# Kernel optimization log

Measured on AMD Instinct MI355X. Metric: run time of the kernel, lower is better.

## Reference

```python
import jax, jax.numpy as jnp
import numpy as np

EMB = 512
N_LAYERS = 8
N_HEADS = 16
FF_MULT = 4
NUM_PATCHES = 196
B = 32
N_VIS = 49
LN_EPS = 1e-5


def _sincos_1d(embed_dim, pos):
    omega = np.arange(embed_dim // 2, dtype=np.float64)
    omega /= embed_dim / 2.0
    omega = 1.0 / 10000 ** omega
    pos = pos.reshape(-1)
    out = np.einsum('m,d->md', pos, omega)
    return np.concatenate([np.sin(out), np.cos(out)], axis=1)


def _sincos_2d(embed_dim, grid_size):
    grid_h = np.arange(grid_size, dtype=np.float32)
    grid_w = np.arange(grid_size, dtype=np.float32)
    grid = np.stack(np.meshgrid(grid_w, grid_h), axis=0).reshape([2, 1, grid_size, grid_size])
    emb_h = _sincos_1d(embed_dim // 2, grid[0])
    emb_w = _sincos_1d(embed_dim // 2, grid[1])
    return np.concatenate([emb_h, emb_w], axis=1)


def setup_inputs() -> dict:
    key = jax.random.key(0)
    ks = jax.random.split(key, 20)
    D, H, FF, L = EMB, N_HEADS, FF_MULT * EMB, N_LAYERS
    s = 0.02
    inp = {}
    inp['x_enc_out_vis'] = jax.random.normal(ks[0], (B, N_VIS + 1, D), dtype=jnp.float32)
    # per-batch permutation of [0, NUM_PATCHES)
    u = jax.random.uniform(ks[1], (B, NUM_PATCHES))
    inp['idx_restore_patches'] = jnp.argsort(u, axis=1).astype(jnp.int32)
    inp['mask_token'] = jax.random.normal(ks[2], (1, 1, D), dtype=jnp.float32) * s
    inp['pos_emb'] = jnp.asarray(_sincos_2d(D, int(NUM_PATCHES ** 0.5))[None], dtype=jnp.float32)
    # stacked per-layer params, layout [in, out] (equivalent to torch Linear math)
    inp['Wq'] = jax.random.normal(ks[3], (L, D, D), dtype=jnp.float32) * s
    inp['bq'] = jnp.zeros((L, D), jnp.float32)
    inp['Wk'] = jax.random.normal(ks[4], (L, D, D), dtype=jnp.float32) * s
    inp['bk'] = jnp.zeros((L, D), jnp.float32)
    inp['Wv'] = jax.random.normal(ks[5], (L, D, D), dtype=jnp.float32) * s
    inp['bv'] = jnp.zeros((L, D), jnp.float32)
    inp['Wo'] = jax.random.normal(ks[6], (L, D, D), dtype=jnp.float32) * s
    inp['bo'] = jnp.zeros((L, D), jnp.float32)
    inp['ln1_g'] = jnp.ones((L, D), jnp.float32)
    inp['ln1_b'] = jnp.zeros((L, D), jnp.float32)
    inp['W1'] = jax.random.normal(ks[7], (L, D, FF), dtype=jnp.float32) * s
    inp['b1'] = jnp.zeros((L, FF), jnp.float32)
    inp['W2'] = jax.random.normal(ks[8], (L, FF, D), dtype=jnp.float32) * s
    inp['b2'] = jnp.zeros((L, D), jnp.float32)
    inp['ln2_g'] = jnp.ones((L, D), jnp.float32)
    inp['ln2_b'] = jnp.zeros((L, D), jnp.float32)
    inp['lnf_g'] = jnp.ones((D,), jnp.float32)
    inp['lnf_b'] = jnp.zeros((D,), jnp.float32)
    return inp


def _layernorm(x, g, b):
    m = jnp.mean(x, axis=-1, keepdims=True)
    v = jnp.mean((x - m) ** 2, axis=-1, keepdims=True)
    return (x - m) * jax.lax.rsqrt(v + LN_EPS) * g + b


def _decoder_forward(x_enc_out_vis, idx_restore, mask_token, pos_emb,
                     Wq, bq, Wk, bk, Wv, bv, Wo, bo, ln1_g, ln1_b,
                     W1, b1, W2, b2, ln2_g, ln2_b, lnf_g, lnf_b):
    Bsz, Nvis1, D = x_enc_out_vis.shape
    N = pos_emb.shape[1]
    H = N_HEADS
    hd = D // H
    # reassemble: visible patches (drop CLS) followed by mask tokens, then unshuffle
    vis = x_enc_out_vis[:, 1:]                                   # [B, Nvis, D]
    mtok = jnp.broadcast_to(mask_token, (Bsz, N - (Nvis1 - 1), D))
    shuffled = jnp.concatenate([vis, mtok], axis=1)              # [B, N, D]
    x = jnp.take_along_axis(shuffled, idx_restore[:, :, None], axis=1) + pos_emb

    def block(x, p):
        wq, bq_, wk, bk_, wv, bv_, wo, bo_, g1, be1, w1, bf1, w2, bf2, g2, be2 = p
        q = (x @ wq + bq_).reshape(Bsz, N, H, hd).transpose(0, 2, 1, 3)
        k = (x @ wk + bk_).reshape(Bsz, N, H, hd).transpose(0, 2, 1, 3)
        v = (x @ wv + bv_).reshape(Bsz, N, H, hd).transpose(0, 2, 1, 3)
        scores = jnp.einsum('bhqd,bhkd->bhqk', q, k) / jnp.sqrt(jnp.float32(hd))
        attn = jax.nn.softmax(scores, axis=-1)
        o = jnp.einsum('bhqk,bhkd->bhqd', attn, v)
        o = o.transpose(0, 2, 1, 3).reshape(Bsz, N, D)
        attended = o @ wo + bo_
        x = _layernorm(attended + x, g1, be1)
        ff = jax.nn.relu(x @ w1 + bf1) @ w2 + bf2
        x = _layernorm(ff + x, g2, be2)
        return x, None

    params = (Wq, bq, Wk, bk, Wv, bv, Wo, bo, ln1_g, ln1_b, W1, b1, W2, b2, ln2_g, ln2_b)
    x, _ = jax.lax.scan(block, x, params)
    return _layernorm(x, lnf_g, lnf_b)


def reference(x_enc_out_vis, idx_restore_patches, mask_token, pos_emb,
              Wq, bq, Wk, bk, Wv, bv, Wo, bo, ln1_g, ln1_b,
              W1, b1, W2, b2, ln2_g, ln2_b, lnf_g, lnf_b):
    return _decoder_forward(x_enc_out_vis, idx_restore_patches, mask_token, pos_emb,
                            Wq, bq, Wk, bk, Wv, bv, Wo, bo, ln1_g, ln1_b,
                            W1, b1, W2, b2, ln2_g, ln2_b, lnf_g, lnf_b)
```

## Files before the change

kernel.cpp:

```cpp
#include <hip/hip_runtime.h>

#define LAYERS 8
#define DIM 512
#define FFD 2048
#define NTOK 6272
#define NSEQ 196
#define BATCH 32
#define NHEAD 16
#define HD 32
#define NP 224
#define PSTRIDE 512

typedef unsigned short u16;
typedef __bf16 bf16x8 __attribute__((ext_vector_type(8)));
typedef float f32x4 __attribute__((ext_vector_type(4)));

__device__ __forceinline__ u16 f2bf(float f) {
    unsigned u = __float_as_uint(f);
    u += 0x7FFF + ((u >> 16) & 1);
    return (u16)(u >> 16);
}

typedef __attribute__((address_space(1))) void gvoid_t;
typedef __attribute__((address_space(3))) void lvoid_t;
__device__ __forceinline__ void gload_lds16(const void* g, void* l) {
    __builtin_amdgcn_global_load_lds((gvoid_t*)g, (lvoid_t*)l, 16, 0, 0);
}

__global__ __launch_bounds__(256) void transpose_w(const float* __restrict__ in,
                                                   u16* __restrict__ out, int K, int N) {
    __shared__ float t[32][33];
    size_t base = (size_t)blockIdx.z * K * N;
    int n0 = blockIdx.x * 32, k0 = blockIdx.y * 32;
    int tx = threadIdx.x, ty = threadIdx.y;
#pragma unroll
    for (int i = 0; i < 4; ++i)
        t[ty + i * 8][tx] = in[base + (size_t)(k0 + ty + i * 8) * N + n0 + tx];
    __syncthreads();
#pragma unroll
    for (int i = 0; i < 4; ++i)
        out[base + (size_t)(n0 + ty + i * 8) * K + k0 + tx] = f2bf(t[tx][ty + i * 8]);
}

__global__ void pack3_bias(const float* __restrict__ a, const float* __restrict__ b,
                           const float* __restrict__ c, float* __restrict__ o, int n) {
    int i = blockIdx.x * 256 + threadIdx.x;
    if (i < n) { o[i] = a[i]; o[n + i] = b[i]; o[2 * n + i] = c[i]; }
}

__global__ __launch_bounds__(128) void gather_pos(const float* __restrict__ xenc,
                                                  const int* __restrict__ idx,
                                                  const float* __restrict__ mtok,
                                                  const float* __restrict__ pos,
                                                  float* __restrict__ x, u16* __restrict__ xb) {
    int token = blockIdx.x;
    int b = token / NSEQ, t = token - b * NSEQ;
    int id = idx[token];
    const float* src = (id < 49) ? (xenc + ((size_t)b * 50 + id + 1) * DIM) : mtok;
    int d = threadIdx.x * 4;
    float4 s = *(const float4*)(src + d);
    float4 p = *(const float4*)(pos + (size_t)t * DIM + d);
    float4 r;
    r.x = s.x + p.x; r.y = s.y + p.y; r.z = s.z + p.z; r.w = s.w + p.w;
    *(float4*)(x + (size_t)token * DIM + d) = r;
    ushort4 rb;
    rb.x = f2bf(r.x); rb.y = f2bf(r.y); rb.z = f2bf(r.z); rb.w = f2bf(r.w);
    *(ushort4*)(xb + (size_t)token * DIM + d) = rb;
}

template<int EPI>
__global__ __launch_bounds__(512) void gemm8(
    const u16* __restrict__ A, int lda, long long zsA,
    const u16* __restrict__ Bt, int ldb, long long zsB,
    const float* __restrict__ bias, long long zsBias,
    float* __restrict__ outF, u16* __restrict__ outB, long long zsOut,
    int N, int K) {
    __shared__ u16 As[128 * 32];
    __shared__ u16 Bs[128 * 32];
    int tid = threadIdx.x;
    int lane = tid & 63, wid = tid >> 6;
    int z = blockIdx.z;
    const u16* Az = A + (size_t)z * zsA;
    const u16* Bz = Bt + (size_t)z * zsB;
    int m0 = blockIdx.y * 128, n0 = blockIdx.x * 128;
    int l16 = lane & 15, kq = lane >> 4;
    int wm = (wid >> 2) * 64, wn = (wid & 3) * 32;
    int arow = tid >> 2, koff0 = (tid & 3) * 16;

    f32x4 acc[4][2];
    f32x4 zero = {0.f, 0.f, 0.f, 0.f};
#pragma unroll
    for (int a = 0; a < 4; ++a)
#pragma unroll
        for (int b = 0; b < 2; ++b) acc[a][b] = zero;

    for (int k0 = 0; k0 < K; k0 += 32) {
        __syncthreads();
        gload_lds16((const char*)Az + ((size_t)(m0 + arow) * lda + k0) * 2 + koff0,
                    (char*)As + (size_t)tid * 16);
        gload_lds16((const char*)Bz + ((size_t)(n0 + arow) * ldb + k0) * 2 + koff0,
                    (char*)Bs + (size_t)tid * 16);
        __syncthreads();

        bf16x8 af[4], bfr[2];
#pragma unroll
        for (int mr = 0; mr < 4; ++mr)
            af[mr] = *(const bf16x8*)&As[(wm + mr * 16 + l16) * 32 + kq * 8];
#pragma unroll
        for (int nc = 0; nc < 2; ++nc)
            bfr[nc] = *(const bf16x8*)&Bs[(wn + nc * 16 + l16) * 32 + kq * 8];
#pragma unroll
        for (int mr = 0; mr < 4; ++mr)
#pragma unroll
            for (int nc = 0; nc < 2; ++nc)
                acc[mr][nc] = __builtin_amdgcn_mfma_f32_16x16x32_bf16(af[mr], bfr[nc],
                                                                      acc[mr][nc], 0, 0, 0);
    }

    const float* biasz = (EPI != 4) ? bias + (size_t)z * zsBias : nullptr;
#pragma unroll
    for (int mr = 0; mr < 4; ++mr)
#pragma unroll
        for (int nc = 0; nc < 2; ++nc)
#pragma unroll
            for (int i = 0; i < 4; ++i) {
                int rg = m0 + wm + mr * 16 + kq * 4 + i;
                int cg = n0 + wn + nc * 16 + l16;
                float v = acc[mr][nc][i];
                size_t off = (size_t)z * zsOut + (size_t)rg * N + cg;
                if (EPI == 1) { v += biasz[cg]; outB[off] = f2bf(v > 0.f ? v : 0.f); }
                else if (EPI == 3) { v += biasz[cg]; outB[off] = f2bf(v); }
                else outF[off] = v;
            }
}

__global__ __launch_bounds__(256) void red_ln(const float* __restrict__ p0, long long ps,
                                              const float* __restrict__ bias,
                                              const float* __restrict__ gg,
                                              const float* __restrict__ bb,
                                              float* __restrict__ x, u16* __restrict__ xb) {
    int t = blockIdx.x * 4 + (threadIdx.x >> 6);
    int lane = threadIdx.x & 63;
    size_t base = (size_t)t * DIM;
    int c0 = lane * 4, c1 = 256 + lane * 4;
    float4 a = *(const float4*)(p0 + base + c0);
    float4 c = *(const float4*)(p0 + base + c1);
    float4 a2 = *(const float4*)(p0 + ps + base + c0);
    float4 c2 = *(const float4*)(p0 + ps + base + c1);
    float4 ba = *(const float4*)(bias + c0);
    float4 bc = *(const float4*)(bias + c1);
    float4 xa = *(const float4*)(x + base + c0);
    float4 xc = *(const float4*)(x + base + c1);
    a.x += a2.x + ba.x + xa.x; a.y += a2.y + ba.y + xa.y;
    a.z += a2.z + ba.z + xa.z; a.w += a2.w + ba.w + xa.w;
    c.x += c2.x + bc.x + xc.x; c.y += c2.y + bc.y + xc.y;
    c.z += c2.z + bc.z + xc.z; c.w += c2.w + bc.w + xc.w;
    float s = a.x + a.y + a.z + a.w + c.x + c.y + c.z + c.w;
    float s2 = a.x * a.x + a.y * a.y + a.z * a.z + a.w * a.w
             + c.x * c.x + c.y * c.y + c.z * c.z + c.w * c.w;
#pragma unroll
    for (int off = 32; off; off >>= 1) { s += __shfl_xor(s, off); s2 += __shfl_xor(s2, off); }
    float m = s * (1.f / 512.f);
    float var = s2 * (1.f / 512.f) - m * m;
    float rs = rsqrtf(var + 1e-5f);
    float4 g0 = *(const float4*)(gg + c0);
    float4 g1 = *(const float4*)(gg + c1);
    float4 b0 = *(const float4*)(bb + c0);
    float4 b1 = *(const float4*)(bb + c1);
    float4 o0, o1;
    o0.x = (a.x - m) * rs * g0.x + b0.x;
    o0.y = (a.y - m) * rs * g0.y + b0.y;
    o0.z = (a.z - m) * rs * g0.z + b0.z;
    o0.w = (a.w - m) * rs * g0.w + b0.w;
    o1.x = (c.x - m) * rs * g1.x + b1.x;
    o1.y = (c.y - m) * rs * g1.y + b1.y;
    o1.z = (c.z - m) * rs * g1.z + b1.z;
    o1.w = (c.w - m) * rs * g1.w + b1.w;
    *(float4*)(x + base + c0) = o0;
    *(float4*)(x + base + c1) = o1;
    ushort4 u0, u1;
    u0.x = f2bf(o0.x); u0.y = f2bf(o0.y); u0.z = f2bf(o0.z); u0.w = f2bf(o0.w);
    u1.x = f2bf(o1.x); u1.y = f2bf(o1.y); u1.z = f2bf(o1.z); u1.w = f2bf(o1.w);
    *(ushort4*)(xb + base + c0) = u0;
    *(ushort4*)(xb + base + c1) = u1;
}

__global__ __launch_bounds__(256) void attn_mfma(const u16* __restrict__ qkvb,
                                                 u16* __restrict__ ob) {
    __shared__ u16 Ks[NP * 32];
    __shared__ u16 VTs[32 * 232];
    __shared__ u16 Ps[4][16 * (PSTRIDE / 2)];
    int bh = blockIdx.x;
    int b = bh >> 4, h = bh & 15;
    int tid = threadIdx.x, lane = tid & 63, wid = tid >> 6;
    int l16 = lane & 15, kq = lane >> 4;
    const size_t MS = (size_t)NTOK * DIM;
    const u16* qg = qkvb + ((size_t)b * NSEQ) * DIM + h * HD;
    const u16* kg = qg + MS;
    const u16* vg = qg + 2 * MS;

    for (int c = tid; c < 784; c += 256) {
        int row = c >> 2, ch = c & 3;
        gload_lds16(kg + (size_t)row * DIM + ch * 8, (char*)Ks + c * 16);
    }
    for (int i = tid; i < 448; i += 256) ((unsigned*)(Ks + 196 * 32))[i] = 0;
    for (int i = tid; i < 1568; i += 256) {
        int j = i >> 3, d0 = (i & 7) * 4;
        ushort4 vv = *(const ushort4*)(vg + (size_t)j * DIM + d0);
        VTs[(d0 + 0) * 232 + j] = vv.x;
        VTs[(d0 + 1) * 232 + j] = vv.y;
        VTs[(d0 + 2) * 232 + j] = vv.z;
        VTs[(d0 + 3) * 232 + j] = vv.w;
    }
    for (int i = tid; i < 1024; i += 256) {
        int d = i >> 5, j = 196 + (i & 31);
        VTs[d * 232 + j] = 0;
    }
    __syncthreads();

    const float scale = 0.17677669529663687f;
    char* psb = (char*)&Ps[wid][0];

    for (int p = wid; p < 13; p += 4) {
        int r0 = p * 16;
        int qrow = r0 + l16; if (qrow > 195) qrow = 195;
        bf16x8 qf = *(const bf16x8*)(qg + (size_t)qrow * DIM + kq * 8);

        f32x4 z4 = {0.f, 0.f, 0.f, 0.f};
        f32x4 s[14];
#pragma unroll
        for (int ct = 0; ct < 14; ++ct) {
            bf16x8 kf = *(const bf16x8*)&Ks[(ct * 16 + l16) * 32 + kq * 8];
            s[ct] = __builtin_amdgcn_mfma_f32_16x16x32_bf16(qf, kf, z4, 0, 0, 0);
        }
        bool v12 = (l16 < 4);
        float mx[4], sum[4], inv[4];
#pragma unroll
        for (int i = 0; i < 4; ++i) {
            float m = -1e30f;
#pragma unroll
            for (int ct = 0; ct < 12; ++ct) m = fmaxf(m, s[ct][i]);
            if (v12) m = fmaxf(m, s[12][i]);
            mx[i] = m * scale;
        }
#pragma unroll
        for (int off = 8; off; off >>= 1)
#pragma unroll
            for (int i = 0; i < 4; ++i) mx[i] = fmaxf(mx[i], __shfl_xor(mx[i], off));
#pragma unroll
        for (int i = 0; i < 4; ++i) sum[i] = 0.f;
#pragma unroll
        for (int ct = 0; ct < 14; ++ct)
#pragma unroll
            for (int i = 0; i < 4; ++i) {
                bool valid = (ct < 12) || (ct == 12 && v12);
                float e = valid ? __expf(s[ct][i] * scale - mx[i]) : 0.f;
                s[ct][i] = e;
                sum[i] += e;
            }
#pragma unroll
        for (int off = 8; off; off >>= 1)
#pragma unroll
            for (int i = 0; i < 4; ++i) sum[i] += __shfl_xor(sum[i], off);
#pragma unroll
        for (int i = 0; i < 4; ++i) inv[i] = 1.f / sum[i];

#pragma unroll
        for (int ct = 0; ct < 14; ++ct)
#pragma unroll
            for (int i = 0; i < 4; ++i) {
                int rl = kq * 4 + i;
                int byte = rl * PSTRIDE + (((ct * 16 + l16) * 2) ^ ((rl & 7) << 4));
                *(u16*)(psb + byte) = f2bf(s[ct][i]);
            }

        f32x4 o0 = {0.f, 0.f, 0.f, 0.f}, o1 = {0.f, 0.f, 0.f, 0.f};
#pragma unroll
        for (int kt = 0; kt < 7; ++kt) {
            int K2 = kt * 64 + kq * 16;
            bf16x8 pa = *(const bf16x8*)(psb + l16 * PSTRIDE + (K2 ^ ((l16 & 7) << 4)));
            bf16x8 va = *(const bf16x8*)&VTs[l16 * 232 + kt * 32 + kq * 8];
            bf16x8 vb = *(const bf16x8*)&VTs[(16 + l16) * 232 + kt * 32 + kq * 8];
            o0 = __builtin_amdgcn_mfma_f32_16x16x32_bf16(pa, va, o0, 0, 0, 0);
            o1 = __builtin_amdgcn_mfma_f32_16x16x32_bf16(pa, vb, o1, 0, 0, 0);
        }
#pragma unroll
        for (int i = 0; i < 4; ++i) {
            int row = r0 + kq * 4 + i;
            if (row < NSEQ) {
                size_t rb = ((size_t)b * NSEQ + row) * DIM + h * HD;
                ob[rb + l16] = f2bf(o0[i] * inv[i]);
                ob[rb + 16 + l16] = f2bf(o1[i] * inv[i]);
            }
        }
    }
}

__global__ __launch_bounds__(256) void ln_final(const float* __restrict__ y,
                                                const float* __restrict__ gg,
                                                const float* __restrict__ bb,
                                                float* __restrict__ xout) {
    int t = blockIdx.x * 4 + (threadIdx.x >> 6);
    int lane = threadIdx.x & 63;
    const float* row = y + (size_t)t * DIM;
    float4 a = *(const float4*)(row + lane * 4);
    float4 c = *(const float4*)(row + 256 + lane * 4);
    float s = a.x + a.y + a.z + a.w + c.x + c.y + c.z + c.w;
    float s2 = a.x * a.x + a.y * a.y + a.z * a.z + a.w * a.w
             + c.x * c.x + c.y * c.y + c.z * c.z + c.w * c.w;
#pragma unroll
    for (int off = 32; off; off >>= 1) { s += __shfl_xor(s, off); s2 += __shfl_xor(s2, off); }
    float m = s * (1.f / 512.f);
    float var = s2 * (1.f / 512.f) - m * m;
    float rs = rsqrtf(var + 1e-5f);
    float4 g0 = *(const float4*)(gg + lane * 4);
    float4 g1 = *(const float4*)(gg + 256 + lane * 4);
    float4 b0 = *(const float4*)(bb + lane * 4);
    float4 b1 = *(const float4*)(bb + 256 + lane * 4);
    float4 o0, o1;
    o0.x = (a.x - m) * rs * g0.x + b0.x;
    o0.y = (a.y - m) * rs * g0.y + b0.y;
    o0.z = (a.z - m) * rs * g0.z + b0.z;
    o0.w = (a.w - m) * rs * g0.w + b0.w;
    o1.x = (c.x - m) * rs * g1.x + b1.x;
    o1.y = (c.y - m) * rs * g1.y + b1.y;
    o1.z = (c.z - m) * rs * g1.z + b1.z;
    o1.w = (c.w - m) * rs * g1.w + b1.w;
    *(float4*)(xout + (size_t)t * DIM + lane * 4) = o0;
    *(float4*)(xout + (size_t)t * DIM + 256 + lane * 4) = o1;
}

extern "C" void kernel_launch(void* const* d_in, const int* in_sizes, int n_in,
                              void* d_out, int out_size, void* d_ws, size_t ws_size,
                              hipStream_t stream) {
    const float* xenc = (const float*)d_in[0];
    const int*   idxr = (const int*)d_in[1];
    const float* mtok = (const float*)d_in[2];
    const float* pos  = (const float*)d_in[3];
    const float* Wq = (const float*)d_in[4];  const float* bq = (const float*)d_in[5];
    const float* Wk = (const float*)d_in[6];  const float* bk = (const float*)d_in[7];
    const float* Wv = (const float*)d_in[8];  const float* bv = (const float*)d_in[9];
    const float* Wo = (const float*)d_in[10]; const float* bo = (const float*)d_in[11];
    const float* ln1g = (const float*)d_in[12]; const float* ln1b = (const float*)d_in[13];
    const float* W1 = (const float*)d_in[14]; const float* b1 = (const float*)d_in[15];
    const float* W2 = (const float*)d_in[16]; const float* b2 = (const float*)d_in[17];
    const float* ln2g = (const float*)d_in[18]; const float* ln2b = (const float*)d_in[19];
    const float* lnfg = (const float*)d_in[20]; const float* lnfb = (const float*)d_in[21];

    char* w = (char*)d_ws;
    u16* WTqkvo = (u16*)w; w += (size_t)4 * LAYERS * DIM * DIM * 2;
    u16* WT1    = (u16*)w; w += (size_t)LAYERS * DIM * FFD * 2;
    u16* WT2    = (u16*)w; w += (size_t)LAYERS * FFD * DIM * 2;
    float* bqkv = (float*)w; w += (size_t)3 * LAYERS * DIM * 4;
    float* x    = (float*)w; w += (size_t)NTOK * DIM * 4;
    u16*   xb   = (u16*)w;  w += (size_t)NTOK * DIM * 2;
    u16*   qkvb = (u16*)w;  w += (size_t)3 * NTOK * DIM * 2;
    u16*   ob   = (u16*)w;  w += (size_t)NTOK * DIM * 2;
    u16*   hb   = (u16*)w;  w += (size_t)NTOK * FFD * 2;
    size_t need = (size_t)(w - (char*)d_ws);
    if (ws_size < need) return;

    float* pj0 = (float*)qkvb;
    float* pj1 = (float*)hb;
    long long zs_proj = (long long)(pj1 - pj0);
    float* ffp = (float*)qkvb;
    const long long ND = (long long)NTOK * DIM;

    const size_t WL = (size_t)DIM * DIM;

    transpose_w<<<dim3(DIM / 32, DIM / 32, LAYERS), dim3(32, 8), 0, stream>>>(Wq, WTqkvo + 0 * (size_t)LAYERS * WL, DIM, DIM);
    transpose_w<<<dim3(DIM / 32, DIM / 32, LAYERS), dim3(32, 8), 0, stream>>>(Wk, WTqkvo + 1 * (size_t)LAYERS * WL, DIM, DIM);
    transpose_w<<<dim3(DIM / 32, DIM / 32, LAYERS), dim3(32, 8), 0, stream>>>(Wv, WTqkvo + 2 * (size_t)LAYERS * WL, DIM, DIM);
    transpose_w<<<dim3(DIM / 32, DIM / 32, LAYERS), dim3(32, 8), 0, stream>>>(Wo, WTqkvo + 3 * (size_t)LAYERS * WL, DIM, DIM);
    transpose_w<<<dim3(FFD / 32, DIM / 32, LAYERS), dim3(32, 8), 0, stream>>>(W1, WT1, DIM, FFD);
    transpose_w<<<dim3(DIM / 32, FFD / 32, LAYERS), dim3(32, 8), 0, stream>>>(W2, WT2, FFD, DIM);
    pack3_bias<<<(LAYERS * DIM + 255) / 256, 256, 0, stream>>>(bq, bk, bv, bqkv, LAYERS * DIM);

    gather_pos<<<NTOK, 128, 0, stream>>>(xenc, idxr, mtok, pos, x, xb);

    for (int l = 0; l < LAYERS; ++l) {
        gemm8<3><<<dim3(4, 49, 3), 512, 0, stream>>>(
            xb, DIM, 0, WTqkvo + l * WL, DIM, (long long)LAYERS * WL,
            bqkv + l * DIM, (long long)LAYERS * DIM,
            nullptr, qkvb, ND, DIM, DIM);
        attn_mfma<<<BATCH * NHEAD, 256, 0, stream>>>(qkvb, ob);
        gemm8<4><<<dim3(4, 49, 2), 512, 0, stream>>>(
            ob, DIM, 256, WTqkvo + 3 * (size_t)LAYERS * WL + l * WL, DIM, 256,
            nullptr, 0, pj0, nullptr, zs_proj, DIM, 256);
        red_ln<<<NTOK / 4, 256, 0, stream>>>(pj0, zs_proj, bo + l * DIM,
                                             ln1g + l * DIM, ln1b + l * DIM, x, xb);
        gemm8<1><<<dim3(16, 49, 1), 512, 0, stream>>>(
            xb, DIM, 0, WT1 + (size_t)l * DIM * FFD, DIM, 0,
            b1 + l * FFD, 0, nullptr, hb, 0, FFD, DIM);
        gemm8<4><<<dim3(4, 49, 2), 512, 0, stream>>>(
            hb, FFD, 1024, WT2 + (size_t)l * FFD * DIM, FFD, 1024,
            nullptr, 0, ffp, nullptr, ND, DIM, 1024);
        red_ln<<<NTOK / 4, 256, 0, stream>>>(ffp, ND, b2 + l * DIM,
                                             ln2g + l * DIM, ln2b + l * DIM, x, xb);
    }
    ln_final<<<NTOK / 4, 256, 0, stream>>>(x, lnfg, lnfb, (float*)d_out);
}
```

Measured before the change: 1.029 ms.

## Use 4-wave 64x64-per-wave GEMM with BK=64, swizzled LDS, and bf16 split-K partials

The GEMM moves from 8 waves of 64x32 tiles with BK=32 to 4 waves of 64x64 tiles with BK=64. This doubles MFMA work per LDS load and halves the number of barriers. An XOR swizzle on the LDS layout is meant to avoid bank conflicts. The split-K partial sums for the output projection and FFN2 are now stored as bf16 instead of fp32, and the reduce+layernorm kernel reads them 8 at a time, which cuts partial-sum traffic at some cost in precision. Register pressure is higher because each thread holds 16 accumulators.

```diff
diff --git a/kernel.cpp b/kernel.cpp
--- a/kernel.cpp
+++ b/kernel.cpp
@@ -14,11 +14,15 @@
 typedef unsigned short u16;
 typedef __bf16 bf16x8 __attribute__((ext_vector_type(8)));
 typedef float f32x4 __attribute__((ext_vector_type(4)));
+typedef unsigned short u16x8 __attribute__((ext_vector_type(8)));
 
 __device__ __forceinline__ u16 f2bf(float f) {
     unsigned u = __float_as_uint(f);
     u += 0x7FFF + ((u >> 16) & 1);
     return (u16)(u >> 16);
+}
+__device__ __forceinline__ float bf2f(u16 u) {
+    return __uint_as_float((unsigned)u << 16);
 }
 
 typedef __attribute__((address_space(1))) void gvoid_t;
@@ -69,14 +73,14 @@
 }
 
 template<int EPI>
-__global__ __launch_bounds__(512) void gemm8(
+__global__ __launch_bounds__(256) void gemm4(
     const u16* __restrict__ A, int lda, long long zsA,
     const u16* __restrict__ Bt, int ldb, long long zsB,
     const float* __restrict__ bias, long long zsBias,
-    float* __restrict__ outF, u16* __restrict__ outB, long long zsOut,
+    u16* __restrict__ outB, long long zsOut,
     int N, int K) {
-    __shared__ u16 As[128 * 32];
-    __shared__ u16 Bs[128 * 32];
+    __shared__ u16 As[128 * 64];
+    __shared__ u16 Bs[128 * 64];
     int tid = threadIdx.x;
     int lane = tid & 63, wid = tid >> 6;
     int z = blockIdx.z;
@@ -84,44 +88,58 @@
     const u16* Bz = Bt + (size_t)z * zsB;
     int m0 = blockIdx.y * 128, n0 = blockIdx.x * 128;
     int l16 = lane & 15, kq = lane >> 4;
-    int wm = (wid >> 2) * 64, wn = (wid & 3) * 32;
-    int arow = tid >> 2, koff0 = (tid & 3) * 16;
-
-    f32x4 acc[4][2];
+    int wm = (wid >> 1) * 64, wn = (wid & 1) * 64;
+
+    f32x4 acc[4][4];
     f32x4 zero = {0.f, 0.f, 0.f, 0.f};
 #pragma unroll
     for (int a = 0; a < 4; ++a)
 #pragma unroll
-        for (int b = 0; b < 2; ++b) acc[a][b] = zero;
-
-    for (int k0 = 0; k0 < K; k0 += 32) {
+        for (int b = 0; b < 4; ++b) acc[a][b] = zero;
+
+    for (int k0 = 0; k0 < K; k0 += 64) {
         __syncthreads();
-        gload_lds16((const char*)Az + ((size_t)(m0 + arow) * lda + k0) * 2 + koff0,
-                    (char*)As + (size_t)tid * 16);
-        gload_lds16((const char*)Bz + ((size_t)(n0 + arow) * ldb + k0) * 2 + koff0,
-                    (char*)Bs + (size_t)tid * 16);
+#pragma unroll
+        for (int i = 0; i < 4; ++i) {
+            int c = i * 256 + tid;
+            int row = c >> 3;
+            int kof = ((c & 7) * 16) ^ ((row & 7) << 4);
+            gload_lds16((const char*)Az + ((size_t)(m0 + row) * lda + k0) * 2 + kof,
+                        (char*)As + (size_t)c * 16);
+            gload_lds16((const char*)Bz + ((size_t)(n0 + row) * ldb + k0) * 2 + kof,
+                        (char*)Bs + (size_t)c * 16);
+        }
         __syncthreads();
 
-        bf16x8 af[4], bfr[2];
-#pragma unroll
-        for (int mr = 0; mr < 4; ++mr)
-            af[mr] = *(const bf16x8*)&As[(wm + mr * 16 + l16) * 32 + kq * 8];
-#pragma unroll
-        for (int nc = 0; nc < 2; ++nc)
-            bfr[nc] = *(const bf16x8*)&Bs[(wn + nc * 16 + l16) * 32 + kq * 8];
-#pragma unroll
-        for (int mr = 0; mr < 4; ++mr)
-#pragma unroll
-            for (int nc = 0; nc < 2; ++nc)
-                acc[mr][nc] = __builtin_amdgcn_mfma_f32_16x16x32_bf16(af[mr], bfr[nc],
-                                                                      acc[mr][nc], 0, 0, 0);
+#pragma unroll
+        for (int kh = 0; kh < 2; ++kh) {
+            bf16x8 af[4], bfr[4];
+#pragma unroll
+            for (int mr = 0; mr < 4; ++mr) {
+                int row = wm + mr * 16 + l16;
+                int cb = (kh * 64 + kq * 16) ^ ((row & 7) << 4);
+                af[mr] = *(const bf16x8*)((const char*)As + row * 128 + cb);
+            }
+#pragma unroll
+            for (int nc = 0; nc < 4; ++nc) {
+                int row = wn + nc * 16 + l16;
+                int cb = (kh * 64 + kq * 16) ^ ((row & 7) << 4);
+                bfr[nc] = *(const bf16x8*)((const char*)Bs + row * 128 + cb);
+            }
+#pragma unroll
+            for (int mr = 0; mr < 4; ++mr)
+#pragma unroll
+                for (int nc = 0; nc < 4; ++nc)
+                    acc[mr][nc] = __builtin_amdgcn_mfma_f32_16x16x32_bf16(af[mr], bfr[nc],
+                                                                          acc[mr][nc], 0, 0, 0);
+        }
     }
 
     const float* biasz = (EPI != 4) ? bias + (size_t)z * zsBias : nullptr;
 #pragma unroll
     for (int mr = 0; mr < 4; ++mr)
 #pragma unroll
-        for (int nc = 0; nc < 2; ++nc)
+        for (int nc = 0; nc < 4; ++nc)
 #pragma unroll
             for (int i = 0; i < 4; ++i) {
                 int rg = m0 + wm + mr * 16 + kq * 4 + i;
@@ -130,11 +148,11 @@
                 size_t off = (size_t)z * zsOut + (size_t)rg * N + cg;
                 if (EPI == 1) { v += biasz[cg]; outB[off] = f2bf(v > 0.f ? v : 0.f); }
                 else if (EPI == 3) { v += biasz[cg]; outB[off] = f2bf(v); }
-                else outF[off] = v;
-            }
-}
-
-__global__ __launch_bounds__(256) void red_ln(const float* __restrict__ p0, long long ps,
+                else outB[off] = f2bf(v);
+            }
+}
+
+__global__ __launch_bounds__(256) void red_ln(const u16* __restrict__ p0, long long ps,
                                               const float* __restrict__ bias,
                                               const float* __restrict__ gg,
                                               const float* __restrict__ bb,
@@ -142,47 +160,45 @@
     int t = blockIdx.x * 4 + (threadIdx.x >> 6);
     int lane = threadIdx.x & 63;
     size_t base = (size_t)t * DIM;
-    int c0 = lane * 4, c1 = 256 + lane * 4;
-    float4 a = *(const float4*)(p0 + base + c0);
-    float4 c = *(const float4*)(p0 + base + c1);
-    float4 a2 = *(const float4*)(p0 + ps + base + c0);
-    float4 c2 = *(const float4*)(p0 + ps + base + c1);
+    int c0 = lane * 8;
+    u16x8 pa = *(const u16x8*)(p0 + base + c0);
+    u16x8 pb = *(const u16x8*)(p0 + ps + base + c0);
+    float4 xa = *(const float4*)(x + base + c0);
+    float4 xc = *(const float4*)(x + base + c0 + 4);
     float4 ba = *(const float4*)(bias + c0);
-    float4 bc = *(const float4*)(bias + c1);
-    float4 xa = *(const float4*)(x + base + c0);
-    float4 xc = *(const float4*)(x + base + c1);
-    a.x += a2.x + ba.x + xa.x; a.y += a2.y + ba.y + xa.y;
-    a.z += a2.z + ba.z + xa.z; a.w += a2.w + ba.w + xa.w;
-    c.x += c2.x + bc.x + xc.x; c.y += c2.y + bc.y + xc.y;
-    c.z += c2.z + bc.z + xc.z; c.w += c2.w + bc.w + xc.w;
-    float s = a.x + a.y + a.z + a.w + c.x + c.y + c.z + c.w;
-    float s2 = a.x * a.x + a.y * a.y + a.z * a.z + a.w * a.w
-             + c.x * c.x + c.y * c.y + c.z * c.z + c.w * c.w;
+    float4 bc = *(const float4*)(bias + c0 + 4);
+    float xs[8] = {xa.x, xa.y, xa.z, xa.w, xc.x, xc.y, xc.z, xc.w};
+    float bs[8] = {ba.x, ba.y, ba.z, ba.w, bc.x, bc.y, bc.z, bc.w};
+    float v[8];
+    float s = 0.f, s2 = 0.f;
+#pragma unroll
+    for (int i = 0; i < 8; ++i) {
+        v[i] = bf2f(pa[i]) + bf2f(pb[i]) + bs[i] + xs[i];
+        s += v[i]; s2 += v[i] * v[i];
+    }
 #pragma unroll
     for (int off = 32; off; off >>= 1) { s += __shfl_xor(s, off); s2 += __shfl_xor(s2, off); }
     float m = s * (1.f / 512.f);
     float var = s2 * (1.f / 512.f) - m * m;
     float rs = rsqrtf(var + 1e-5f);
-    float4 g0 = *(const float4*)(gg + c0);
-    float4 g1 = *(const float4*)(gg + c1);
+    float4 ga = *(const float4*)(gg + c0);
+    float4 gc = *(const float4*)(gg + c0 + 4);
     float4 b0 = *(const float4*)(bb + c0);
-    float4 b1 = *(const float4*)(bb + c1);
-    float4 o0, o1;
-    o0.x = (a.x - m) * rs * g0.x + b0.x;
-    o0.y = (a.y - m) * rs * g0.y + b0.y;
-    o0.z = (a.z - m) * rs * g0.z + b0.z;
-    o0.w = (a.w - m) * rs * g0.w + b0.w;
-    o1.x = (c.x - m) * rs * g1.x + b1.x;
-    o1.y = (c.y - m) * rs * g1.y + b1.y;
-    o1.z = (c.z - m) * rs * g1.z + b1.z;
-    o1.w = (c.w - m) * rs * g1.w + b1.w;
+    float4 b1 = *(const float4*)(bb + c0 + 4);
+    float gs[8] = {ga.x, ga.y, ga.z, ga.w, gc.x, gc.y, gc.z, gc.w};
+    float os[8] = {b0.x, b0.y, b0.z, b0.w, b1.x, b1.y, b1.z, b1.w};
+    float o[8];
+    u16x8 ob16;
+#pragma unroll
+    for (int i = 0; i < 8; ++i) {
+        o[i] = (v[i] - m) * rs * gs[i] + os[i];
+        ob16[i] = f2bf(o[i]);
+    }
+    float4 o0 = {o[0], o[1], o[2], o[3]};
+    float4 o1 = {o[4], o[5], o[6], o[7]};
     *(float4*)(x + base + c0) = o0;
-    *(float4*)(x + base + c1) = o1;
-    ushort4 u0, u1;
-    u0.x = f2bf(o0.x); u0.y = f2bf(o0.y); u0.z = f2bf(o0.z); u0.w = f2bf(o0.w);
-    u1.x = f2bf(o1.x); u1.y = f2bf(o1.y); u1.z = f2bf(o1.z); u1.w = f2bf(o1.w);
-    *(ushort4*)(xb + base + c0) = u0;
-    *(ushort4*)(xb + base + c1) = u1;
+    *(float4*)(x + base + c0 + 4) = o1;
+    *(u16x8*)(xb + base + c0) = ob16;
 }
 
 __global__ __launch_bounds__(256) void attn_mfma(const u16* __restrict__ qkvb,
@@ -360,10 +376,7 @@
     size_t need = (size_t)(w - (char*)d_ws);
     if (ws_size < need) return;
 
-    float* pj0 = (float*)qkvb;
-    float* pj1 = (float*)hb;
-    long long zs_proj = (long long)(pj1 - pj0);
-    float* ffp = (float*)qkvb;
+    u16* pp = qkvb;
     const long long ND = (long long)NTOK * DIM;
 
     const size_t WL = (size_t)DIM * DIM;
@@ -379,23 +392,23 @@
     gather_pos<<<NTOK, 128, 0, stream>>>(xenc, idxr, mtok, pos, x, xb);
 
     for (int l = 0; l < LAYERS; ++l) {
-        gemm8<3><<<dim3(4, 49, 3), 512, 0, stream>>>(
+        gemm4<3><<<dim3(4, 49, 3), 256, 0, stream>>>(
             xb, DIM, 0, WTqkvo + l * WL, DIM, (long long)LAYERS * WL,
             bqkv + l * DIM, (long long)LAYERS * DIM,
-            nullptr, qkvb, ND, DIM, DIM);
+            qkvb, ND, DIM, DIM);
         attn_mfma<<<BATCH * NHEAD, 256, 0, stream>>>(qkvb, ob);
-        gemm8<4><<<dim3(4, 49, 2), 512, 0, stream>>>(
+        gemm4<4><<<dim3(4, 49, 2), 256, 0, stream>>>(
             ob, DIM, 256, WTqkvo + 3 * (size_t)LAYERS * WL + l * WL, DIM, 256,
-            nullptr, 0, pj0, nullptr, zs_proj, DIM, 256);
-        red_ln<<<NTOK / 4, 256, 0, stream>>>(pj0, zs_proj, bo + l * DIM,
+            nullptr, 0, pp, ND, DIM, 256);
+        red_ln<<<NTOK / 4, 256, 0, stream>>>(pp, ND, bo + l * DIM,
                                              ln1g + l * DIM, ln1b + l * DIM, x, xb);
-        gemm8<1><<<dim3(16, 49, 1), 512, 0, stream>>>(
+        gemm4<1><<<dim3(16, 49, 1), 256, 0, stream>>>(
             xb, DIM, 0, WT1 + (size_t)l * DIM * FFD, DIM, 0,
-            b1 + l * FFD, 0, nullptr, hb, 0, FFD, DIM);
-        gemm8<4><<<dim3(4, 49, 2), 512, 0, stream>>>(
+            b1 + l * FFD, 0, hb, 0, FFD, DIM);
+        gemm4<4><<<dim3(4, 49, 2), 256, 0, stream>>>(
             hb, FFD, 1024, WT2 + (size_t)l * FFD * DIM, FFD, 1024,
-            nullptr, 0, ffp, nullptr, ND, DIM, 1024);
-        red_ln<<<NTOK / 4, 256, 0, stream>>>(ffp, ND, b2 + l * DIM,
+            nullptr, 0, pp, ND, DIM, 1024);
+        red_ln<<<NTOK / 4, 256, 0, stream>>>(pp, ND, b2 + l * DIM,
                                              ln2g + l * DIM, ln2b + l * DIM, x, xb);
     }
     ln_final<<<NTOK / 4, 256, 0, stream>>>(x, lnfg, lnfb, (float*)d_out);
```

Result: no change. 1.011 ms (-1.8%).
